# Optimization experiments

Hardware: AMD Instinct MI355X
Metric: run time of the kernel (lower is better)

## Reference

```python
import jax, jax.numpy as jnp
import numpy as np

B, T, VOCAB = 65536, 34, 14
D_MODEL, TOK_DIM, POS_DIM, QK_DIM, FFN = 5, 2, 3, 5, 2
MAX_DIGITS = 10
EPS = 1e-5


def setup_inputs() -> dict:
    key = jax.random.key(0)
    ks = jax.random.split(key, 8)
    return dict(
        idx=jax.random.randint(ks[0], (B, T), 0, VOCAB),
        tok_A=jnp.float32(2.5), tok_start=jnp.float32(-1.2), tok_stride=jnp.float32(0.29),
        sp_amp=jnp.float32(3.5), sp_phase=jnp.float32(0.0), sp_slope=jnp.float32(0.15), sp_offset=jnp.float32(0.0),
        norm_w=jnp.ones((D_MODEL,), jnp.float32),
        q_w=jax.random.normal(ks[1], (QK_DIM, POS_DIM), jnp.float32) * 0.5,
        q_phase=jnp.zeros((1,), jnp.float32),
        out_A=jax.random.normal(ks[2], (D_MODEL, 1), jnp.float32) * 0.45,
        out_B=jax.random.normal(ks[3], (1, D_MODEL), jnp.float32) * 0.2,
        fc1_w=jax.random.normal(ks[4], (FFN, D_MODEL), jnp.float32) * 0.4,
        fc2_w=jax.random.normal(ks[5], (D_MODEL, FFN), jnp.float32) * 0.4,
        head_w=jax.random.normal(ks[6], (TOK_DIM, D_MODEL), jnp.float32) * 0.4,
    )


def rmsnorm(x, w):
    rms = jnp.sqrt(jnp.mean(x * x, axis=-1, keepdims=True) + EPS)
    return x / rms * w


def micro_forward(idx, tok_A, tok_start, tok_stride, sp_amp, sp_phase, sp_slope, sp_offset,
                  norm_w, q_w, q_phase, out_A, out_B, fc1_w, fc2_w, head_w):
    # token arc embedding table (V, 2)
    d = jnp.arange(VOCAB, dtype=jnp.float32)
    ang = tok_start + d * tok_stride
    tok_emb = jnp.stack([tok_A * jnp.cos(ang), tok_A * jnp.sin(ang)], axis=-1)
    # spiral positional embedding (T, 3)
    t = jnp.arange(T, dtype=jnp.float32)
    th = 2.0 * jnp.pi * t / MAX_DIGITS + sp_phase
    pos = jnp.stack([sp_amp * jnp.cos(th), sp_amp * jnp.sin(th), sp_slope * t + sp_offset], axis=-1)
    # embed: concat token (B,T,2) + position (T,3) -> (B,T,5)
    x = jnp.concatenate([tok_emb[idx], jnp.broadcast_to(pos, (idx.shape[0], T, POS_DIM))], axis=-1)
    # attention (pre-norm); q/k from positions only (qk_input='pos'), shared across batch
    h = rmsnorm(x, norm_w)
    k = pos @ q_w.T                       # (T, QK)
    c, s = jnp.cos(q_phase[0]), jnp.sin(q_phase[0])
    q = k.at[:, 0].set(c * k[:, 0] - s * k[:, 1]).at[:, 1].set(s * k[:, 0] + c * k[:, 1])
    scores = (q @ k.T) / jnp.sqrt(jnp.float32(QK_DIM))   # (T, T)
    causal = jnp.tril(jnp.ones((T, T), bool))
    attn = jax.nn.softmax(jnp.where(causal, scores, -1e9), axis=-1)
    attn_out = jnp.einsum('ts,bsd->btd', attn, h)         # v = normed x (head_dim = d_model)
    x = x + (attn_out @ out_A) @ out_B                    # rank-1 out_proj, residual
    # FFN (pre-norm, 2 hidden units)
    h2 = rmsnorm(x, norm_w)
    x = x + jax.nn.relu(h2 @ fc1_w.T) @ fc2_w.T
    # head: project to token plane, read out against arc embedding table
    hf = rmsnorm(x, norm_w)
    logits = (hf @ head_w.T) @ tok_emb.T                  # (B, T, V)
    return logits


def reference(idx, tok_A, tok_start, tok_stride, sp_amp, sp_phase, sp_slope, sp_offset,
              norm_w, q_w, q_phase, out_A, out_B, fc1_w, fc2_w, head_w):
    return micro_forward(idx, tok_A, tok_start, tok_stride, sp_amp, sp_phase, sp_slope, sp_offset,
                         norm_w, q_w, q_phase, out_A, out_B, fc1_w, fc2_w, head_w)
```

## Files before the change

### kernel.cpp

```cpp
#include <hip/hip_runtime.h>
#include <math.h>

#define T 34
#define V 14
#define NT 256
#define NBLK 2176
#define NWAVES 8704
#define KTILES 4
#define LIM (65536 * 34)


__global__ void setup_k(const float* __restrict__ tokA_p, const float* __restrict__ tokStart_p,
                        const float* __restrict__ tokStride_p, const float* __restrict__ spAmp_p,
                        const float* __restrict__ spPhase_p, const float* __restrict__ spSlope_p,
                        const float* __restrict__ spOffset_p, const float* __restrict__ norm_w,
                        const float* __restrict__ q_w, const float* __restrict__ q_phase,
                        const float* __restrict__ out_A, float* __restrict__ ws)
{
    __shared__ float sPOS[T][3];
    __shared__ float sK[T][5];
    __shared__ float sQ[T][5];
    __shared__ float sTE[V][2];
    __shared__ float sA[T][35];

    const int tid = threadIdx.x;

    if (tid < V) {
        float ang = tokStart_p[0] + (float)tid * tokStride_p[0];
        float c = tokA_p[0] * cosf(ang), s = tokA_p[0] * sinf(ang);
        sTE[tid][0] = c; sTE[tid][1] = s;
        ws[1680 + 2 * tid] = c; ws[1681 + 2 * tid] = s;
    }
    if (tid < T) {
        float th = (float)tid * 0.62831853071795864769f + spPhase_p[0];
        float p0 = spAmp_p[0] * cosf(th), p1 = spAmp_p[0] * sinf(th);
        float p2 = spSlope_p[0] * (float)tid + spOffset_p[0];
        sPOS[tid][0] = p0; sPOS[tid][1] = p1; sPOS[tid][2] = p2;
        ws[1708 + 3 * tid] = p0; ws[1709 + 3 * tid] = p1; ws[1710 + 3 * tid] = p2;
        float kk[5];
        #pragma unroll
        for (int i = 0; i < 5; ++i)
            kk[i] = p0 * q_w[3 * i] + p1 * q_w[3 * i + 1] + p2 * q_w[3 * i + 2];
        float cc = cosf(q_phase[0]), ss = sinf(q_phase[0]);
        #pragma unroll
        for (int i = 0; i < 5; ++i) sK[tid][i] = kk[i];
        sQ[tid][0] = cc * kk[0] - ss * kk[1];
        sQ[tid][1] = ss * kk[0] + cc * kk[1];
        sQ[tid][2] = kk[2]; sQ[tid][3] = kk[3]; sQ[tid][4] = kk[4];
    }
    __syncthreads();

    if (tid < T) {
        const int t = tid;
        float mx = -1e30f;
        for (int s = 0; s <= t; ++s) {
            float d = (sQ[t][0] * sK[s][0] + sQ[t][1] * sK[s][1] + sQ[t][2] * sK[s][2]
                     + sQ[t][3] * sK[s][3] + sQ[t][4] * sK[s][4]) * 0.44721359549995793928f;
            sA[t][s] = d;
            mx = fmaxf(mx, d);
        }
        float sum = 0.f;
        for (int s = 0; s <= t; ++s) { float e = expf(sA[t][s] - mx); sA[t][s] = e; sum += e; }
        float inv = 1.f / sum;
        for (int s = 0; s < 35; ++s) ws[t * 35 + s] = (s <= t) ? sA[t][s] * inv : 0.f;
    }
    for (int e = tid; e < 490; e += 64) {
        int v = e / 35, s = e - v * 35;
        float g = 0.f;
        if (s < T) {
            float x0 = sTE[v][0], x1 = sTE[v][1];
            float x2 = sPOS[s][0], x3 = sPOS[s][1], x4 = sPOS[s][2];
            float ms = (x0*x0 + x1*x1 + x2*x2 + x3*x3 + x4*x4) * 0.2f;
            float r = rsqrtf(ms + 1e-5f);
            g = (x0 * norm_w[0] * out_A[0] + x1 * norm_w[1] * out_A[1]
               + x2 * norm_w[2] * out_A[2] + x3 * norm_w[3] * out_A[3]
               + x4 * norm_w[4] * out_A[4]) * r;
        }
        ws[1190 + e] = g;
    }
}

__global__ __launch_bounds__(NT, 4) void micro_main(
    const int* __restrict__ idx, const float* __restrict__ ws, float* __restrict__ out,
    const float* __restrict__ norm_w, const float* __restrict__ out_B,
    const float* __restrict__ fc1_w, const float* __restrict__ fc2_w,
    const float* __restrict__ head_w)
{
    __shared__ float G_lds[V * 35];
    __shared__ float TE_lds[V * 2];
    __shared__ float gbW[4][104];
    __shared__ float stageAll[4 * 896];

    const int tid = threadIdx.x;
    const int w = tid >> 6, lane = tid & 63;
    const int wid = blockIdx.x * 4 + w;

    for (int i = tid; i < 490; i += NT) G_lds[i] = ws[1190 + i];
    if (tid < 28) TE_lds[tid] = ws[1680 + tid];
    for (int i = tid; i < 1190; i += NT) stageAll[i] = ws[i];
    __syncthreads();

    const int t = (wid * 64 + lane) % T;
    float A[T];
    #pragma unroll
    for (int s = 0; s < T; ++s) A[s] = stageAll[t * 35 + s];
    const float ps0 = ws[1708 + 3 * t], ps1 = ws[1709 + 3 * t], ps2 = ws[1710 + 3 * t];
    __syncthreads();

    const float nw0 = norm_w[0], nw1 = norm_w[1], nw2 = norm_w[2], nw3 = norm_w[3], nw4 = norm_w[4];
    const float oB0 = out_B[0], oB1 = out_B[1], oB2 = out_B[2], oB3 = out_B[3], oB4 = out_B[4];
    float w1[2][5], hw[2][5], w20[5], w21[5];
    #pragma unroll
    for (int j = 0; j < 2; ++j)
        #pragma unroll
        for (int d = 0; d < 5; ++d) { w1[j][d] = fc1_w[j*5+d]; hw[j][d] = head_w[j*5+d]; }
    #pragma unroll
    for (int d = 0; d < 5; ++d) { w20[d] = fc2_w[2*d]; w21[d] = fc2_w[2*d+1]; }
    float te0[V], te1[V];
    #pragma unroll
    for (int v = 0; v < V; ++v) { te0[v] = ws[1680 + 2*v]; te1[v] = ws[1681 + 2*v]; }

    const int s_a = (lane < T) ? lane : lane - T;
    const int i2 = lane + 64;
    const int s_b = (i2 < 68) ? i2 - 34 : i2 - 68;
    const bool act2 = (i2 < 102);

    float* gb = gbW[w];
    float* stg = stageAll + w * 896;
    float2* stg2 = reinterpret_cast<float2*>(stg);
    const float4* st4 = reinterpret_cast<const float4*>(stg);

    int tile = wid;
    int b0 = (tile * 64) / T;
    int tk0 = idx[b0 * T + lane];
    int tk1 = idx[min(b0 * T + lane + 64, LIM - 1)];
    int tko = idx[tile * 64 + lane];

    #pragma unroll
    for (int k = 0; k < KTILES; ++k) {
        gb[lane] = G_lds[tk0 * 35 + s_a];
        if (act2) gb[i2] = G_lds[tk1 * 35 + s_b];

        const int item = tile * 64 + lane;
        const int b = item / T;
        const int rbase = (b - b0) * T;
        const int curtok = tko;
        const int tile_n = tile + NWAVES;

        if (k < KTILES - 1) {
            int b0n = (tile_n * 64) / T;
            tk0 = idx[b0n * T + lane];
            tk1 = idx[min(b0n * T + lane + 64, LIM - 1)];
            tko = idx[tile_n * 64 + lane];
            b0 = b0n;
        }

        float acc = 0.f;
        const float2* gbp = reinterpret_cast<const float2*>(gb + rbase);
        #pragma unroll
        for (int s = 0; s < 17; ++s) {
            float2 gg = gbp[s];
            acc = fmaf(A[2*s], gg.x, acc);
            acc = fmaf(A[2*s+1], gg.y, acc);
        }

        float2 te = *reinterpret_cast<const float2*>(&TE_lds[curtok * 2]);
        float x0 = te.x + acc * oB0;
        float x1 = te.y + acc * oB1;
        float x2 = ps0 + acc * oB2;
        float x3 = ps1 + acc * oB3;
        float x4 = ps2 + acc * oB4;

        float ms = (x0*x0 + x1*x1 + x2*x2 + x3*x3 + x4*x4) * 0.2f;
        float rr = rsqrtf(ms + 1e-5f);
        float h0 = x0*rr*nw0, h1 = x1*rr*nw1, h2 = x2*rr*nw2, h3 = x3*rr*nw3, h4 = x4*rr*nw4;
        float f0 = fmaxf(0.f, h0*w1[0][0] + h1*w1[0][1] + h2*w1[0][2] + h3*w1[0][3] + h4*w1[0][4]);
        float f1 = fmaxf(0.f, h0*w1[1][0] + h1*w1[1][1] + h2*w1[1][2] + h3*w1[1][3] + h4*w1[1][4]);
        x0 += f0*w20[0] + f1*w21[0];
        x1 += f0*w20[1] + f1*w21[1];
        x2 += f0*w20[2] + f1*w21[2];
        x3 += f0*w20[3] + f1*w21[3];
        x4 += f0*w20[4] + f1*w21[4];

        ms = (x0*x0 + x1*x1 + x2*x2 + x3*x3 + x4*x4) * 0.2f;
        rr = rsqrtf(ms + 1e-5f);
        h0 = x0*rr*nw0; h1 = x1*rr*nw1; h2 = x2*rr*nw2; h3 = x3*rr*nw3; h4 = x4*rr*nw4;
        float p0 = h0*hw[0][0] + h1*hw[0][1] + h2*hw[0][2] + h3*hw[0][3] + h4*hw[0][4];
        float p1 = h0*hw[1][0] + h1*hw[1][1] + h2*hw[1][2] + h3*hw[1][3] + h4*hw[1][4];

        #pragma unroll
        for (int j = 0; j < 7; ++j) {
            float2 o2;
            o2.x = p0 * te0[2*j]   + p1 * te1[2*j];
            o2.y = p0 * te0[2*j+1] + p1 * te1[2*j+1];
            stg2[lane * 7 + j] = o2;
        }

        float4* outp = reinterpret_cast<float4*>(out) + (size_t)tile * 224;
        outp[lane]       = st4[lane];
        outp[lane + 64]  = st4[lane + 64];
        outp[lane + 128] = st4[lane + 128];
        if (lane < 32) outp[lane + 192] = st4[lane + 192];

        tile = tile_n;
    }
}

extern "C" void kernel_launch(void* const* d_in, const int* in_sizes, int n_in,
                              void* d_out, int out_size, void* d_ws, size_t ws_size,
                              hipStream_t stream) {
    const int*   idx        = (const int*)  d_in[0];
    const float* tok_A      = (const float*)d_in[1];
    const float* tok_start  = (const float*)d_in[2];
    const float* tok_stride = (const float*)d_in[3];
    const float* sp_amp     = (const float*)d_in[4];
    const float* sp_phase   = (const float*)d_in[5];
    const float* sp_slope   = (const float*)d_in[6];
    const float* sp_offset  = (const float*)d_in[7];
    const float* norm_w     = (const float*)d_in[8];
    const float* q_w        = (const float*)d_in[9];
    const float* q_phase    = (const float*)d_in[10];
    const float* out_A      = (const float*)d_in[11];
    const float* out_B      = (const float*)d_in[12];
    const float* fc1_w      = (const float*)d_in[13];
    const float* fc2_w      = (const float*)d_in[14];
    const float* head_w     = (const float*)d_in[15];
    float* out = (float*)d_out;
    float* ws  = (float*)d_ws;

    setup_k<<<1, 64, 0, stream>>>(tok_A, tok_start, tok_stride, sp_amp, sp_phase,
                                  sp_slope, sp_offset, norm_w, q_w, q_phase, out_A, ws);
    micro_main<<<NBLK, NT, 0, stream>>>(idx, ws, out, norm_w, out_B, fc1_w, fc2_w, head_w);
}
```

Measured before the change: 40.65 us.

## Fuse setup kernel into main kernel, recomputing constant tables per block

Removes the separate single-block setup kernel and its global workspace round trip. Each block of the main kernel now computes the token embedding, positional embedding, causal attention matrix and the G table directly into shared memory before processing its tiles. This drops one kernel launch and the serialized tiny-kernel latency. In exchange every block redoes the setup arithmetic, including a serial softmax over up to 34 positions per thread, which lengthens each block's prologue.

```diff
diff --git a/kernel.cpp b/kernel.cpp
--- a/kernel.cpp
+++ b/kernel.cpp
@@ -9,102 +9,91 @@
 #define KTILES 4
 #define LIM (65536 * 34)
 
-
-__global__ void setup_k(const float* __restrict__ tokA_p, const float* __restrict__ tokStart_p,
-                        const float* __restrict__ tokStride_p, const float* __restrict__ spAmp_p,
-                        const float* __restrict__ spPhase_p, const float* __restrict__ spSlope_p,
-                        const float* __restrict__ spOffset_p, const float* __restrict__ norm_w,
-                        const float* __restrict__ q_w, const float* __restrict__ q_phase,
-                        const float* __restrict__ out_A, float* __restrict__ ws)
+__global__ __launch_bounds__(NT, 4) void micro_main(
+    const int* __restrict__ idx, float* __restrict__ out,
+    const float* __restrict__ p_tokA, const float* __restrict__ p_tokStart,
+    const float* __restrict__ p_tokStride, const float* __restrict__ p_spAmp,
+    const float* __restrict__ p_spPhase, const float* __restrict__ p_spSlope,
+    const float* __restrict__ p_spOffset, const float* __restrict__ norm_w,
+    const float* __restrict__ q_w, const float* __restrict__ q_phase,
+    const float* __restrict__ out_A, const float* __restrict__ out_B,
+    const float* __restrict__ fc1_w, const float* __restrict__ fc2_w,
+    const float* __restrict__ head_w)
 {
-    __shared__ float sPOS[T][3];
-    __shared__ float sK[T][5];
-    __shared__ float sQ[T][5];
-    __shared__ float sTE[V][2];
-    __shared__ float sA[T][35];
+    __shared__ float G_lds[V * 35];
+    __shared__ float TE_lds[V * 2];
+    __shared__ float POS_lds[T][3];
+    __shared__ float gbW[4][104];
+    __shared__ float stageAll[4 * 896];
 
     const int tid = threadIdx.x;
+    const int w = tid >> 6, lane = tid & 63;
+    const int wid = blockIdx.x * 4 + w;
+
+    float* sA  = stageAll;
+    float* sKp = stageAll + 1200;
+    float* sQp = stageAll + 1400;
 
     if (tid < V) {
-        float ang = tokStart_p[0] + (float)tid * tokStride_p[0];
-        float c = tokA_p[0] * cosf(ang), s = tokA_p[0] * sinf(ang);
-        sTE[tid][0] = c; sTE[tid][1] = s;
-        ws[1680 + 2 * tid] = c; ws[1681 + 2 * tid] = s;
+        float ang = p_tokStart[0] + (float)tid * p_tokStride[0];
+        TE_lds[2 * tid]     = p_tokA[0] * cosf(ang);
+        TE_lds[2 * tid + 1] = p_tokA[0] * sinf(ang);
     }
     if (tid < T) {
-        float th = (float)tid * 0.62831853071795864769f + spPhase_p[0];
-        float p0 = spAmp_p[0] * cosf(th), p1 = spAmp_p[0] * sinf(th);
-        float p2 = spSlope_p[0] * (float)tid + spOffset_p[0];
-        sPOS[tid][0] = p0; sPOS[tid][1] = p1; sPOS[tid][2] = p2;
-        ws[1708 + 3 * tid] = p0; ws[1709 + 3 * tid] = p1; ws[1710 + 3 * tid] = p2;
+        float th = (float)tid * 0.62831853071795864769f + p_spPhase[0];
+        float p0 = p_spAmp[0] * cosf(th), p1 = p_spAmp[0] * sinf(th);
+        float p2 = p_spSlope[0] * (float)tid + p_spOffset[0];
+        POS_lds[tid][0] = p0; POS_lds[tid][1] = p1; POS_lds[tid][2] = p2;
         float kk[5];
         #pragma unroll
         for (int i = 0; i < 5; ++i)
             kk[i] = p0 * q_w[3 * i] + p1 * q_w[3 * i + 1] + p2 * q_w[3 * i + 2];
         float cc = cosf(q_phase[0]), ss = sinf(q_phase[0]);
         #pragma unroll
-        for (int i = 0; i < 5; ++i) sK[tid][i] = kk[i];
-        sQ[tid][0] = cc * kk[0] - ss * kk[1];
-        sQ[tid][1] = ss * kk[0] + cc * kk[1];
-        sQ[tid][2] = kk[2]; sQ[tid][3] = kk[3]; sQ[tid][4] = kk[4];
+        for (int i = 0; i < 5; ++i) sKp[tid * 5 + i] = kk[i];
+        sQp[tid * 5 + 0] = cc * kk[0] - ss * kk[1];
+        sQp[tid * 5 + 1] = ss * kk[0] + cc * kk[1];
+        sQp[tid * 5 + 2] = kk[2]; sQp[tid * 5 + 3] = kk[3]; sQp[tid * 5 + 4] = kk[4];
     }
     __syncthreads();
 
     if (tid < T) {
         const int t = tid;
+        float q0 = sQp[t*5], q1 = sQp[t*5+1], q2 = sQp[t*5+2], q3 = sQp[t*5+3], q4 = sQp[t*5+4];
+        float sc[T];
         float mx = -1e30f;
         for (int s = 0; s <= t; ++s) {
-            float d = (sQ[t][0] * sK[s][0] + sQ[t][1] * sK[s][1] + sQ[t][2] * sK[s][2]
-                     + sQ[t][3] * sK[s][3] + sQ[t][4] * sK[s][4]) * 0.44721359549995793928f;
-            sA[t][s] = d;
+            float d = (q0 * sKp[s*5] + q1 * sKp[s*5+1] + q2 * sKp[s*5+2]
+                     + q3 * sKp[s*5+3] + q4 * sKp[s*5+4]) * 0.44721359549995793928f;
+            sc[s] = d;
             mx = fmaxf(mx, d);
         }
         float sum = 0.f;
-        for (int s = 0; s <= t; ++s) { float e = expf(sA[t][s] - mx); sA[t][s] = e; sum += e; }
+        for (int s = 0; s <= t; ++s) { float e = expf(sc[s] - mx); sc[s] = e; sum += e; }
         float inv = 1.f / sum;
-        for (int s = 0; s < 35; ++s) ws[t * 35 + s] = (s <= t) ? sA[t][s] * inv : 0.f;
-    }
-    for (int e = tid; e < 490; e += 64) {
+        for (int s = 0; s < 35; ++s) sA[t * 35 + s] = (s <= t && s < T) ? sc[s] * inv : 0.f;
+    }
+    for (int e = tid; e < V * 35; e += NT) {
         int v = e / 35, s = e - v * 35;
         float g = 0.f;
         if (s < T) {
-            float x0 = sTE[v][0], x1 = sTE[v][1];
-            float x2 = sPOS[s][0], x3 = sPOS[s][1], x4 = sPOS[s][2];
+            float x0 = TE_lds[2*v], x1 = TE_lds[2*v+1];
+            float x2 = POS_lds[s][0], x3 = POS_lds[s][1], x4 = POS_lds[s][2];
             float ms = (x0*x0 + x1*x1 + x2*x2 + x3*x3 + x4*x4) * 0.2f;
             float r = rsqrtf(ms + 1e-5f);
             g = (x0 * norm_w[0] * out_A[0] + x1 * norm_w[1] * out_A[1]
                + x2 * norm_w[2] * out_A[2] + x3 * norm_w[3] * out_A[3]
                + x4 * norm_w[4] * out_A[4]) * r;
         }
-        ws[1190 + e] = g;
-    }
-}
-
-__global__ __launch_bounds__(NT, 4) void micro_main(
-    const int* __restrict__ idx, const float* __restrict__ ws, float* __restrict__ out,
-    const float* __restrict__ norm_w, const float* __restrict__ out_B,
-    const float* __restrict__ fc1_w, const float* __restrict__ fc2_w,
-    const float* __restrict__ head_w)
-{
-    __shared__ float G_lds[V * 35];
-    __shared__ float TE_lds[V * 2];
-    __shared__ float gbW[4][104];
-    __shared__ float stageAll[4 * 896];
-
-    const int tid = threadIdx.x;
-    const int w = tid >> 6, lane = tid & 63;
-    const int wid = blockIdx.x * 4 + w;
-
-    for (int i = tid; i < 490; i += NT) G_lds[i] = ws[1190 + i];
-    if (tid < 28) TE_lds[tid] = ws[1680 + tid];
-    for (int i = tid; i < 1190; i += NT) stageAll[i] = ws[i];
+        G_lds[e] = g;
+    }
     __syncthreads();
 
     const int t = (wid * 64 + lane) % T;
     float A[T];
     #pragma unroll
-    for (int s = 0; s < T; ++s) A[s] = stageAll[t * 35 + s];
-    const float ps0 = ws[1708 + 3 * t], ps1 = ws[1709 + 3 * t], ps2 = ws[1710 + 3 * t];
+    for (int s = 0; s < T; ++s) A[s] = sA[t * 35 + s];
+    const float ps0 = POS_lds[t][0], ps1 = POS_lds[t][1], ps2 = POS_lds[t][2];
     __syncthreads();
 
     const float nw0 = norm_w[0], nw1 = norm_w[1], nw2 = norm_w[2], nw3 = norm_w[3], nw4 = norm_w[4];
@@ -118,7 +107,7 @@
     for (int d = 0; d < 5; ++d) { w20[d] = fc2_w[2*d]; w21[d] = fc2_w[2*d+1]; }
     float te0[V], te1[V];
     #pragma unroll
-    for (int v = 0; v < V; ++v) { te0[v] = ws[1680 + 2*v]; te1[v] = ws[1681 + 2*v]; }
+    for (int v = 0; v < V; ++v) { te0[v] = TE_lds[2*v]; te1[v] = TE_lds[2*v+1]; }
 
     const int s_a = (lane < T) ? lane : lane - T;
     const int i2 = lane + 64;
@@ -226,9 +215,9 @@
     const float* fc2_w      = (const float*)d_in[14];
     const float* head_w     = (const float*)d_in[15];
     float* out = (float*)d_out;
-    float* ws  = (float*)d_ws;
-
-    setup_k<<<1, 64, 0, stream>>>(tok_A, tok_start, tok_stride, sp_amp, sp_phase,
-                                  sp_slope, sp_offset, norm_w, q_w, q_phase, out_A, ws);
-    micro_main<<<NBLK, NT, 0, stream>>>(idx, ws, out, norm_w, out_B, fc1_w, fc2_w, head_w);
+
+    micro_main<<<NBLK, NT, 0, stream>>>(idx, out, tok_A, tok_start, tok_stride,
+                                        sp_amp, sp_phase, sp_slope, sp_offset,
+                                        norm_w, q_w, q_phase, out_A, out_B,
+                                        fc1_w, fc2_w, head_w);
 }
```

Result: slower. 68.79 us (+69.2%).

## Interleave two tiles per iteration, nontemporal output stores, drop LDS staging of A

Applied to the files above, without the earlier changes.

Restructures the per-wave loop so that two tiles are processed per iteration, with separate gather buffers and index prefetch for both. This raises memory-level parallelism and instruction overlap. The output writes become nontemporal stores to avoid polluting the cache with the large logits stream. The A matrix is now read straight from global memory instead of being staged through LDS, which removes a block barrier. The dot product is split into two accumulators to shorten the dependency chain, at the cost of more registers and slightly different summation order.

```diff
diff --git a/kernel.cpp b/kernel.cpp
--- a/kernel.cpp
+++ b/kernel.cpp
@@ -6,8 +6,9 @@
 #define NT 256
 #define NBLK 2176
 #define NWAVES 8704
-#define KTILES 4
 #define LIM (65536 * 34)
+
+typedef float f32x4 __attribute__((ext_vector_type(4)));
 
 
 __global__ void setup_k(const float* __restrict__ tokA_p, const float* __restrict__ tokStart_p,
@@ -88,7 +89,7 @@
 {
     __shared__ float G_lds[V * 35];
     __shared__ float TE_lds[V * 2];
-    __shared__ float gbW[4][104];
+    __shared__ float gbW[4][2][104];
     __shared__ float stageAll[4 * 896];
 
     const int tid = threadIdx.x;
@@ -97,15 +98,13 @@
 
     for (int i = tid; i < 490; i += NT) G_lds[i] = ws[1190 + i];
     if (tid < 28) TE_lds[tid] = ws[1680 + tid];
-    for (int i = tid; i < 1190; i += NT) stageAll[i] = ws[i];
     __syncthreads();
 
     const int t = (wid * 64 + lane) % T;
     float A[T];
     #pragma unroll
-    for (int s = 0; s < T; ++s) A[s] = stageAll[t * 35 + s];
+    for (int s = 0; s < T; ++s) A[s] = ws[t * 35 + s];
     const float ps0 = ws[1708 + 3 * t], ps1 = ws[1709 + 3 * t], ps2 = ws[1710 + 3 * t];
-    __syncthreads();
 
     const float nw0 = norm_w[0], nw1 = norm_w[1], nw2 = norm_w[2], nw3 = norm_w[3], nw4 = norm_w[4];
     const float oB0 = out_B[0], oB1 = out_B[1], oB2 = out_B[2], oB3 = out_B[3], oB4 = out_B[4];
@@ -125,44 +124,22 @@
     const int s_b = (i2 < 68) ? i2 - 34 : i2 - 68;
     const bool act2 = (i2 < 102);
 
-    float* gb = gbW[w];
+    float* gbA = gbW[w][0];
+    float* gbB = gbW[w][1];
     float* stg = stageAll + w * 896;
     float2* stg2 = reinterpret_cast<float2*>(stg);
-    const float4* st4 = reinterpret_cast<const float4*>(stg);
-
-    int tile = wid;
-    int b0 = (tile * 64) / T;
-    int tk0 = idx[b0 * T + lane];
-    int tk1 = idx[min(b0 * T + lane + 64, LIM - 1)];
-    int tko = idx[tile * 64 + lane];
-
-    #pragma unroll
-    for (int k = 0; k < KTILES; ++k) {
-        gb[lane] = G_lds[tk0 * 35 + s_a];
-        if (act2) gb[i2] = G_lds[tk1 * 35 + s_b];
-
-        const int item = tile * 64 + lane;
-        const int b = item / T;
-        const int rbase = (b - b0) * T;
-        const int curtok = tko;
-        const int tile_n = tile + NWAVES;
-
-        if (k < KTILES - 1) {
-            int b0n = (tile_n * 64) / T;
-            tk0 = idx[b0n * T + lane];
-            tk1 = idx[min(b0n * T + lane + 64, LIM - 1)];
-            tko = idx[tile_n * 64 + lane];
-            b0 = b0n;
-        }
-
-        float acc = 0.f;
-        const float2* gbp = reinterpret_cast<const float2*>(gb + rbase);
+    const f32x4* st4 = reinterpret_cast<const f32x4*>(stg);
+
+    auto computeItem = [&](int tile, int rbase, int curtok, const float* gbT) {
+        float acc0 = 0.f, acc1 = 0.f;
+        const float2* gbp = reinterpret_cast<const float2*>(gbT + rbase);
         #pragma unroll
         for (int s = 0; s < 17; ++s) {
             float2 gg = gbp[s];
-            acc = fmaf(A[2*s], gg.x, acc);
-            acc = fmaf(A[2*s+1], gg.y, acc);
-        }
+            acc0 = fmaf(A[2*s],   gg.x, acc0);
+            acc1 = fmaf(A[2*s+1], gg.y, acc1);
+        }
+        float acc = acc0 + acc1;
 
         float2 te = *reinterpret_cast<const float2*>(&TE_lds[curtok * 2]);
         float x0 = te.x + acc * oB0;
@@ -195,14 +172,48 @@
             o2.y = p0 * te0[2*j+1] + p1 * te1[2*j+1];
             stg2[lane * 7 + j] = o2;
         }
-
-        float4* outp = reinterpret_cast<float4*>(out) + (size_t)tile * 224;
-        outp[lane]       = st4[lane];
-        outp[lane + 64]  = st4[lane + 64];
-        outp[lane + 128] = st4[lane + 128];
-        if (lane < 32) outp[lane + 192] = st4[lane + 192];
-
-        tile = tile_n;
+        f32x4* outp = reinterpret_cast<f32x4*>(out) + (size_t)tile * 224;
+        __builtin_nontemporal_store(st4[lane],       outp + lane);
+        __builtin_nontemporal_store(st4[lane + 64],  outp + lane + 64);
+        __builtin_nontemporal_store(st4[lane + 128], outp + lane + 128);
+        if (lane < 32)
+            __builtin_nontemporal_store(st4[lane + 192], outp + lane + 192);
+    };
+
+    int tileA = wid, tileB = wid + NWAVES;
+    int b0A = (tileA * 64) / T, b0B = (tileB * 64) / T;
+    int tk0A = idx[b0A * T + lane];
+    int tk1A = idx[min(b0A * T + lane + 64, LIM - 1)];
+    int tkoA = idx[tileA * 64 + lane];
+    int tk0B = idx[b0B * T + lane];
+    int tk1B = idx[min(b0B * T + lane + 64, LIM - 1)];
+    int tkoB = idx[tileB * 64 + lane];
+
+    #pragma unroll
+    for (int it = 0; it < 2; ++it) {
+        gbA[lane] = G_lds[tk0A * 35 + s_a];
+        if (act2) gbA[i2] = G_lds[tk1A * 35 + s_b];
+        gbB[lane] = G_lds[tk0B * 35 + s_a];
+        if (act2) gbB[i2] = G_lds[tk1B * 35 + s_b];
+
+        const int rbA = ((tileA * 64 + lane) / T - b0A) * T;
+        const int rbB = ((tileB * 64 + lane) / T - b0B) * T;
+        const int ctA = tkoA, ctB = tkoB;
+        const int tA = tileA, tB = tileB;
+
+        if (it == 0) {
+            tileA += 2 * NWAVES; tileB += 2 * NWAVES;
+            b0A = (tileA * 64) / T; b0B = (tileB * 64) / T;
+            tk0A = idx[b0A * T + lane];
+            tk1A = idx[min(b0A * T + lane + 64, LIM - 1)];
+            tkoA = idx[tileA * 64 + lane];
+            tk0B = idx[b0B * T + lane];
+            tk1B = idx[min(b0B * T + lane + 64, LIM - 1)];
+            tkoB = idx[tileB * 64 + lane];
+        }
+
+        computeItem(tA, rbA, ctA, gbA);
+        computeItem(tB, rbB, ctB, gbB);
     }
 }
 
```

Measured after the change: 39.57 us. 2.7% less time.

## Split each item across two half-waves and shrink per-tile registers and LDS

Applied to the files above, without the earlier changes.

Each wave now handles 32 items per tile rather than 64. The two half-waves each compute half of the 34-term attention dot product and half of the 14 logits, and combine the partial sums with a cross-lane shuffle. Attention rows are padded to 36 and read from global memory as float4 instead of being staged through LDS, and token ids are cached in LDS. The per-thread register arrays shrink, the min-occupancy hint on launch bounds is dropped, and KTILES is doubled so the grid still covers every item. Output uses nontemporal stores, and a full-wave shuffle is added on each tile's critical path.

```diff
diff --git a/kernel.cpp b/kernel.cpp
--- a/kernel.cpp
+++ b/kernel.cpp
@@ -6,8 +6,10 @@
 #define NT 256
 #define NBLK 2176
 #define NWAVES 8704
-#define KTILES 4
+#define KTILES 8
 #define LIM (65536 * 34)
+
+typedef float f32x4 __attribute__((ext_vector_type(4)));
 
 
 __global__ void setup_k(const float* __restrict__ tokA_p, const float* __restrict__ tokStart_p,
@@ -29,14 +31,16 @@
         float ang = tokStart_p[0] + (float)tid * tokStride_p[0];
         float c = tokA_p[0] * cosf(ang), s = tokA_p[0] * sinf(ang);
         sTE[tid][0] = c; sTE[tid][1] = s;
-        ws[1680 + 2 * tid] = c; ws[1681 + 2 * tid] = s;
+        ws[1728 + 2 * tid] = c; ws[1729 + 2 * tid] = s;
+        ws[1756 + tid] = c;
+        ws[1770 + tid] = s;
     }
     if (tid < T) {
         float th = (float)tid * 0.62831853071795864769f + spPhase_p[0];
         float p0 = spAmp_p[0] * cosf(th), p1 = spAmp_p[0] * sinf(th);
         float p2 = spSlope_p[0] * (float)tid + spOffset_p[0];
         sPOS[tid][0] = p0; sPOS[tid][1] = p1; sPOS[tid][2] = p2;
-        ws[1708 + 3 * tid] = p0; ws[1709 + 3 * tid] = p1; ws[1710 + 3 * tid] = p2;
+        ws[1784 + 3 * tid] = p0; ws[1785 + 3 * tid] = p1; ws[1786 + 3 * tid] = p2;
         float kk[5];
         #pragma unroll
         for (int i = 0; i < 5; ++i)
@@ -62,10 +66,11 @@
         float sum = 0.f;
         for (int s = 0; s <= t; ++s) { float e = expf(sA[t][s] - mx); sA[t][s] = e; sum += e; }
         float inv = 1.f / sum;
-        for (int s = 0; s < 35; ++s) ws[t * 35 + s] = (s <= t) ? sA[t][s] * inv : 0.f;
-    }
-    for (int e = tid; e < 490; e += 64) {
-        int v = e / 35, s = e - v * 35;
+        for (int s = 0; s < 36; ++s)
+            ws[t * 36 + s] = (s <= t) ? sA[t][s] * inv : 0.f;
+    }
+    for (int e = tid; e < V * 36; e += 64) {
+        int v = e / 36, s = e - v * 36;
         float g = 0.f;
         if (s < T) {
             float x0 = sTE[v][0], x1 = sTE[v][1];
@@ -76,97 +81,103 @@
                + x2 * norm_w[2] * out_A[2] + x3 * norm_w[3] * out_A[3]
                + x4 * norm_w[4] * out_A[4]) * r;
         }
-        ws[1190 + e] = g;
+        ws[1224 + e] = g;
     }
 }
 
-__global__ __launch_bounds__(NT, 4) void micro_main(
+__global__ __launch_bounds__(NT) void micro_main(
     const int* __restrict__ idx, const float* __restrict__ ws, float* __restrict__ out,
     const float* __restrict__ norm_w, const float* __restrict__ out_B,
     const float* __restrict__ fc1_w, const float* __restrict__ fc2_w,
     const float* __restrict__ head_w)
 {
-    __shared__ float G_lds[V * 35];
+    __shared__ float G_lds[V * 36];
     __shared__ float TE_lds[V * 2];
-    __shared__ float gbW[4][104];
-    __shared__ float stageAll[4 * 896];
+    __shared__ float gbuf[4][72];
+    __shared__ int   tokb[4][68];
+    __shared__ float stg[4][448];
 
     const int tid = threadIdx.x;
     const int w = tid >> 6, lane = tid & 63;
+    const int li = lane & 31, hi = lane >> 5;
     const int wid = blockIdx.x * 4 + w;
 
-    for (int i = tid; i < 490; i += NT) G_lds[i] = ws[1190 + i];
-    if (tid < 28) TE_lds[tid] = ws[1680 + tid];
-    for (int i = tid; i < 1190; i += NT) stageAll[i] = ws[i];
+    for (int i = tid; i < V * 36; i += NT) G_lds[i] = ws[1224 + i];
+    if (tid < 28) TE_lds[tid] = ws[1728 + tid];
     __syncthreads();
 
-    const int t = (wid * 64 + lane) % T;
-    float A[T];
-    #pragma unroll
-    for (int s = 0; s < T; ++s) A[s] = stageAll[t * 35 + s];
-    const float ps0 = ws[1708 + 3 * t], ps1 = ws[1709 + 3 * t], ps2 = ws[1710 + 3 * t];
-    __syncthreads();
+    const int t = (wid * 32 + li) % T;
+
+    const float* ap = ws + t * 36 + 16 * hi;
+    const float4* ap4 = reinterpret_cast<const float4*>(ap);
+    float4 Aa = ap4[0], Ab = ap4[1], Ac = ap4[2], Ad = ap4[3];
+    float2 Ae = *reinterpret_cast<const float2*>(ap + 16);
+    if (hi == 0) { Ae.x = 0.f; Ae.y = 0.f; }
+
+    const float ps0 = ws[1784 + 3 * t], ps1 = ws[1785 + 3 * t], ps2 = ws[1786 + 3 * t];
 
     const float nw0 = norm_w[0], nw1 = norm_w[1], nw2 = norm_w[2], nw3 = norm_w[3], nw4 = norm_w[4];
     const float oB0 = out_B[0], oB1 = out_B[1], oB2 = out_B[2], oB3 = out_B[3], oB4 = out_B[4];
-    float w1[2][5], hw[2][5], w20[5], w21[5];
+    const float w100 = fc1_w[0], w101 = fc1_w[1], w102 = fc1_w[2], w103 = fc1_w[3], w104 = fc1_w[4];
+    const float w110 = fc1_w[5], w111 = fc1_w[6], w112 = fc1_w[7], w113 = fc1_w[8], w114 = fc1_w[9];
+    const float hw00 = head_w[0], hw01 = head_w[1], hw02 = head_w[2], hw03 = head_w[3], hw04 = head_w[4];
+    const float hw10 = head_w[5], hw11 = head_w[6], hw12 = head_w[7], hw13 = head_w[8], hw14 = head_w[9];
+    const float w200 = fc2_w[0], w201 = fc2_w[1];
+    const float w210 = fc2_w[2], w211 = fc2_w[3];
+    const float w220 = fc2_w[4], w221 = fc2_w[5];
+    const float w230 = fc2_w[6], w231 = fc2_w[7];
+    const float w240 = fc2_w[8], w241 = fc2_w[9];
+
+    float t0s[7], t1s[7];
     #pragma unroll
-    for (int j = 0; j < 2; ++j)
-        #pragma unroll
-        for (int d = 0; d < 5; ++d) { w1[j][d] = fc1_w[j*5+d]; hw[j][d] = head_w[j*5+d]; }
-    #pragma unroll
-    for (int d = 0; d < 5; ++d) { w20[d] = fc2_w[2*d]; w21[d] = fc2_w[2*d+1]; }
-    float te0[V], te1[V];
-    #pragma unroll
-    for (int v = 0; v < V; ++v) { te0[v] = ws[1680 + 2*v]; te1[v] = ws[1681 + 2*v]; }
-
-    const int s_a = (lane < T) ? lane : lane - T;
-    const int i2 = lane + 64;
-    const int s_b = (i2 < 68) ? i2 - 34 : i2 - 68;
-    const bool act2 = (i2 < 102);
-
-    float* gb = gbW[w];
-    float* stg = stageAll + w * 896;
-    float2* stg2 = reinterpret_cast<float2*>(stg);
-    const float4* st4 = reinterpret_cast<const float4*>(stg);
+    for (int m = 0; m < 7; ++m) {
+        t0s[m] = hi ? ws[1756 + 7 + m] : ws[1756 + m];
+        t1s[m] = hi ? ws[1770 + 7 + m] : ws[1770 + m];
+    }
 
     int tile = wid;
-    int b0 = (tile * 64) / T;
-    int tk0 = idx[b0 * T + lane];
-    int tk1 = idx[min(b0 * T + lane + 64, LIM - 1)];
-    int tko = idx[tile * 64 + lane];
-
-    #pragma unroll
     for (int k = 0; k < KTILES; ++k) {
-        gb[lane] = G_lds[tk0 * 35 + s_a];
-        if (act2) gb[i2] = G_lds[tk1 * 35 + s_b];
-
-        const int item = tile * 64 + lane;
-        const int b = item / T;
-        const int rbase = (b - b0) * T;
-        const int curtok = tko;
-        const int tile_n = tile + NWAVES;
-
-        if (k < KTILES - 1) {
-            int b0n = (tile_n * 64) / T;
-            tk0 = idx[b0n * T + lane];
-            tk1 = idx[min(b0n * T + lane + 64, LIM - 1)];
-            tko = idx[tile_n * 64 + lane];
-            b0 = b0n;
+        const int b0 = (int)((unsigned)(tile * 32) / 34u);
+        const int base = b0 * T;
+
+        {
+            int tk = idx[min(base + lane, LIM - 1)];
+            int s = (lane < T) ? lane : lane - T;
+            int slot = (lane < T) ? lane : lane + 2;
+            gbuf[w][slot] = G_lds[tk * 36 + s];
+            tokb[w][lane] = tk;
+            if (lane < 4) {
+                int j2 = 64 + lane;
+                int tk2 = idx[min(base + j2, LIM - 1)];
+                gbuf[w][j2 + 2] = G_lds[tk2 * 36 + (j2 - T)];
+                tokb[w][j2] = tk2;
+            }
         }
 
-        float acc = 0.f;
-        const float2* gbp = reinterpret_cast<const float2*>(gb + rbase);
-        #pragma unroll
-        for (int s = 0; s < 17; ++s) {
-            float2 gg = gbp[s];
-            acc = fmaf(A[2*s], gg.x, acc);
-            acc = fmaf(A[2*s+1], gg.y, acc);
-        }
-
-        float2 te = *reinterpret_cast<const float2*>(&TE_lds[curtok * 2]);
-        float x0 = te.x + acc * oB0;
-        float x1 = te.y + acc * oB1;
+        const int j_own = tile * 32 + li - base;
+        const int r = (j_own >= T) ? 1 : 0;
+
+        const float* gp = &gbuf[w][r * 36 + 16 * hi];
+        const float4* gp4 = reinterpret_cast<const float4*>(gp);
+        float4 g0 = gp4[0], g1 = gp4[1], g2 = gp4[2], g3 = gp4[3];
+        float2 g4 = *reinterpret_cast<const float2*>(gp + 16);
+        float a0 = 0.f, a1 = 0.f;
+        a0 = fmaf(Aa.x, g0.x, a0); a1 = fmaf(Aa.y, g0.y, a1);
+        a0 = fmaf(Aa.z, g0.z, a0); a1 = fmaf(Aa.w, g0.w, a1);
+        a0 = fmaf(Ab.x, g1.x, a0); a1 = fmaf(Ab.y, g1.y, a1);
+        a0 = fmaf(Ab.z, g1.z, a0); a1 = fmaf(Ab.w, g1.w, a1);
+        a0 = fmaf(Ac.x, g2.x, a0); a1 = fmaf(Ac.y, g2.y, a1);
+        a0 = fmaf(Ac.z, g2.z, a0); a1 = fmaf(Ac.w, g2.w, a1);
+        a0 = fmaf(Ad.x, g3.x, a0); a1 = fmaf(Ad.y, g3.y, a1);
+        a0 = fmaf(Ad.z, g3.z, a0); a1 = fmaf(Ad.w, g3.w, a1);
+        a0 = fmaf(Ae.x, g4.x, a0); a1 = fmaf(Ae.y, g4.y, a1);
+        float acc = a0 + a1;
+        acc += __shfl_xor(acc, 32);
+
+        int tok_own = tokb[w][j_own];
+        float2 tet = *reinterpret_cast<const float2*>(&TE_lds[tok_own * 2]);
+        float x0 = tet.x + acc * oB0;
+        float x1 = tet.y + acc * oB1;
         float x2 = ps0 + acc * oB2;
         float x3 = ps1 + acc * oB3;
         float x4 = ps2 + acc * oB4;
@@ -174,35 +185,32 @@
         float ms = (x0*x0 + x1*x1 + x2*x2 + x3*x3 + x4*x4) * 0.2f;
         float rr = rsqrtf(ms + 1e-5f);
         float h0 = x0*rr*nw0, h1 = x1*rr*nw1, h2 = x2*rr*nw2, h3 = x3*rr*nw3, h4 = x4*rr*nw4;
-        float f0 = fmaxf(0.f, h0*w1[0][0] + h1*w1[0][1] + h2*w1[0][2] + h3*w1[0][3] + h4*w1[0][4]);
-        float f1 = fmaxf(0.f, h0*w1[1][0] + h1*w1[1][1] + h2*w1[1][2] + h3*w1[1][3] + h4*w1[1][4]);
-        x0 += f0*w20[0] + f1*w21[0];
-        x1 += f0*w20[1] + f1*w21[1];
-        x2 += f0*w20[2] + f1*w21[2];
-        x3 += f0*w20[3] + f1*w21[3];
-        x4 += f0*w20[4] + f1*w21[4];
+        float f0 = fmaxf(0.f, h0*w100 + h1*w101 + h2*w102 + h3*w103 + h4*w104);
+        float f1 = fmaxf(0.f, h0*w110 + h1*w111 + h2*w112 + h3*w113 + h4*w114);
+        x0 += f0*w200 + f1*w201;
+        x1 += f0*w210 + f1*w211;
+        x2 += f0*w220 + f1*w221;
+        x3 += f0*w230 + f1*w231;
+        x4 += f0*w240 + f1*w241;
 
         ms = (x0*x0 + x1*x1 + x2*x2 + x3*x3 + x4*x4) * 0.2f;
         rr = rsqrtf(ms + 1e-5f);
         h0 = x0*rr*nw0; h1 = x1*rr*nw1; h2 = x2*rr*nw2; h3 = x3*rr*nw3; h4 = x4*rr*nw4;
-        float p0 = h0*hw[0][0] + h1*hw[0][1] + h2*hw[0][2] + h3*hw[0][3] + h4*hw[0][4];
-        float p1 = h0*hw[1][0] + h1*hw[1][1] + h2*hw[1][2] + h3*hw[1][3] + h4*hw[1][4];
-
+        float p0 = h0*hw00 + h1*hw01 + h2*hw02 + h3*hw03 + h4*hw04;
+        float p1 = h0*hw10 + h1*hw11 + h2*hw12 + h3*hw13 + h4*hw14;
+
+        float* sp = &stg[w][li * 14 + 7 * hi];
         #pragma unroll
-        for (int j = 0; j < 7; ++j) {
-            float2 o2;
-            o2.x = p0 * te0[2*j]   + p1 * te1[2*j];
-            o2.y = p0 * te0[2*j+1] + p1 * te1[2*j+1];
-            stg2[lane * 7 + j] = o2;
-        }
-
-        float4* outp = reinterpret_cast<float4*>(out) + (size_t)tile * 224;
-        outp[lane]       = st4[lane];
-        outp[lane + 64]  = st4[lane + 64];
-        outp[lane + 128] = st4[lane + 128];
-        if (lane < 32) outp[lane + 192] = st4[lane + 192];
-
-        tile = tile_n;
+        for (int m = 0; m < 7; ++m)
+            sp[m] = fmaf(p1, t1s[m], p0 * t0s[m]);
+
+        const f32x4* s4 = reinterpret_cast<const f32x4*>(stg[w]);
+        f32x4* op = reinterpret_cast<f32x4*>(out) + (size_t)tile * 112;
+        __builtin_nontemporal_store(s4[lane], op + lane);
+        if (lane < 48)
+            __builtin_nontemporal_store(s4[64 + lane], op + 64 + lane);
+
+        tile += NWAVES;
     }
 }
 
```

Measured after the change: 40.76 us. About the same (+0.3%).
